# Kernel optimization log

Hardware: AMD Instinct MI355X
Metric: run time of the kernel (lower is better)

The kernel has to match this reference:

```python
import jax, jax.numpy as jnp
import numpy as np

N = 100000   # nodes
E = 600000   # edges
D = 128      # hidden_dim
R = 8        # edge_vocab_size (num_relations)
B = 64       # graphs in batch
V = 5000     # node_vocab_size
L = 3        # num_layers


def setup_inputs() -> dict:
    key = jax.random.key(0)
    ks = jax.random.split(key, 16)
    s = 1.0 / np.sqrt(D)
    node_type = jax.random.randint(ks[0], (N,), 0, V, dtype=jnp.int32)
    edge_index = jax.random.randint(ks[1], (2, E), 0, N, dtype=jnp.int32)
    edge_type = jax.random.randint(ks[2], (E,), 0, R, dtype=jnp.int32)
    batch = jnp.sort(jax.random.randint(ks[3], (N,), 0, B, dtype=jnp.int32))
    node_emb = jax.random.normal(ks[4], (V, D), dtype=jnp.float32)
    rel_w = jax.random.normal(ks[5], (L, R, D, D), dtype=jnp.float32) * s
    root_w = jax.random.normal(ks[6], (L, D, D), dtype=jnp.float32) * s
    bias = jnp.zeros((L, D), dtype=jnp.float32)
    risk_w1 = jax.random.normal(ks[7], (D, D), dtype=jnp.float32) * s
    risk_b1 = jnp.zeros((D,), dtype=jnp.float32)
    risk_w2 = jax.random.normal(ks[8], (D, 1), dtype=jnp.float32) * s
    risk_b2 = jnp.zeros((1,), dtype=jnp.float32)
    safe_w1 = jax.random.normal(ks[9], (D, D), dtype=jnp.float32) * s
    safe_b1 = jnp.zeros((D,), dtype=jnp.float32)
    safe_w2 = jax.random.normal(ks[10], (D, 1), dtype=jnp.float32) * s
    safe_b2 = jnp.zeros((1,), dtype=jnp.float32)
    return dict(node_type=node_type, edge_index=edge_index, edge_type=edge_type,
                batch=batch, node_emb=node_emb, rel_w=rel_w, root_w=root_w,
                bias=bias, risk_w1=risk_w1, risk_b1=risk_b1, risk_w2=risk_w2,
                risk_b2=risk_b2, safe_w1=safe_w1, safe_b1=safe_b1,
                safe_w2=safe_w2, safe_b2=safe_b2)


def _rgcn_layer(x, edge_index, edge_type, Wrel, Wroot, b):
    # PyG RGCNConv: per-relation mean aggregation of source features,
    # then relation-specific linear + root transform + bias.
    src, dst = edge_index[0], edge_index[1]
    seg = dst * R + edge_type                      # combined (node, relation) id
    msgs = x[src]                                  # [E, D] gather
    sums = jax.ops.segment_sum(msgs, seg, num_segments=N * R)      # [N*R, D]
    cnt = jax.ops.segment_sum(jnp.ones((E,), x.dtype), seg, num_segments=N * R)
    mean = sums / jnp.maximum(cnt, 1.0)[:, None]
    mean = mean.reshape(N, R, D)
    out = jnp.einsum('nrd,rde->ne', mean, Wrel) + x @ Wroot + b
    return out


def _mlp_head(g, w1, b1, w2, b2):
    h = jax.nn.relu(g @ w1 + b1)
    return (h @ w2 + b2).squeeze(-1)               # dropout is identity in eval


def reference(node_type, edge_index, edge_type, batch, node_emb, rel_w, root_w,
              bias, risk_w1, risk_b1, risk_w2, risk_b2, safe_w1, safe_b1,
              safe_w2, safe_b2):
    x = node_emb[node_type]                        # [N, D]
    for l in range(L):                             # fixed small layer loop
        x = jax.nn.relu(_rgcn_layer(x, edge_index, edge_type,
                                    rel_w[l], root_w[l], bias[l]))
    # global_mean_pool over graph ids
    g_sum = jax.ops.segment_sum(x, batch, num_segments=B)          # [B, D]
    g_cnt = jax.ops.segment_sum(jnp.ones((N,), x.dtype), batch, num_segments=B)
    g = g_sum / jnp.maximum(g_cnt, 1.0)[:, None]
    risk_pred = _mlp_head(g, risk_w1, risk_b1, risk_w2, risk_b2)   # [B]
    safe_logit = _mlp_head(g, safe_w1, safe_b1, safe_w2, safe_b2)  # [B]
    return risk_pred, safe_logit
```

## Files before the change

### kernel.cpp

```cpp
#include <hip/hip_runtime.h>
#include <hip/hip_bf16.h>

#define N_NODES 100000
#define N_EDGES 600000
#define DIM     128
#define N_REL   8
#define N_GRAPH 64
#define N_LAYER 3
#define NR      (N_NODES * N_REL)
#define NB1     782

typedef __attribute__((ext_vector_type(4))) float float4v;
typedef __attribute__((ext_vector_type(2))) float float2v;
typedef unsigned long long ull;

__device__ __forceinline__ int gswz8(int row, int g) {
    return row * 16 + (g ^ (row & 15));
}

#define W8_TOTAL (N_LAYER * 9 * 8192)
#define PB_HIST  2344
#define PB_GATH  12500
#define PB_WPRE  864
#define PB_BCNT  1
#define PB_TOTAL (PB_HIST + PB_GATH + PB_WPRE + PB_BCNT)

__global__ __launch_bounds__(256) void k_prep(
    const int* __restrict__ ei, const int* __restrict__ et, int* __restrict__ counts,
    const int* __restrict__ nt, const float* __restrict__ emb, unsigned int* __restrict__ x8,
    const float* __restrict__ relw, const float* __restrict__ rootw,
    unsigned short* __restrict__ W8,
    const int* __restrict__ batch, int* __restrict__ gcnt)
{
    const int b = blockIdx.x, t = threadIdx.x;
    if (b < PB_HIST) {
        int e = b * 256 + t;
        if (e < N_EDGES) {
            int seg = ei[N_EDGES + e] * N_REL + et[e];
            atomicAdd(&counts[seg], 1);
        }
    } else if (b < PB_HIST + PB_GATH) {
        int gid = (b - PB_HIST) * 256 + t;
        int n = gid >> 5, up = gid & 31;
        const float* row = emb + (size_t)nt[n] * DIM;
        int p0 = up * 4;
        float f0 = row[((p0 + 0) & 7) * 16 + ((p0 + 0) >> 3)];
        float f1 = row[((p0 + 1) & 7) * 16 + ((p0 + 1) >> 3)];
        float f2 = row[((p0 + 2) & 7) * 16 + ((p0 + 2) >> 3)];
        float f3 = row[((p0 + 3) & 7) * 16 + ((p0 + 3) >> 3)];
        int u = __builtin_amdgcn_cvt_pk_fp8_f32(f0, f1, 0, false);
        u = __builtin_amdgcn_cvt_pk_fp8_f32(f2, f3, u, true);
        x8[gid] = (unsigned int)u;
    } else if (b < PB_HIST + PB_GATH + PB_WPRE) {
        int gid = (b - PB_HIST - PB_GATH) * 256 + t;
        int l = gid / (9 * 8192);
        int rem = gid - l * 9 * 8192;
        int r = rem >> 13;
        int idx = rem & 8191;
        int n = idx >> 6, p2 = idx & 63;
        int pos0 = 2 * p2, pos1 = 2 * p2 + 1;
        int k0 = (pos0 & 7) * 16 + (pos0 >> 3);
        int k1 = (pos1 & 7) * 16 + (pos1 >> 3);
        float w0, w1;
        if (r < 8) {
            const float* base = relw + ((size_t)(l * 8 + r) * 128) * 128 + n;
            w0 = base[(size_t)k0 * 128];
            w1 = base[(size_t)k1 * 128];
        } else {
            const float* base = rootw + (size_t)l * 128 * 128 + n;
            w0 = base[(size_t)k0 * 128];
            w1 = base[(size_t)k1 * 128];
        }
        int pk = __builtin_amdgcn_cvt_pk_fp8_f32(w0, w1, 0, false);
        W8[gid] = (unsigned short)(pk & 0xffff);
    } else {
        int g = t;
        if (g < N_GRAPH) {
            int lo = 0, hi = N_NODES;
            while (lo < hi) { int mid = (lo + hi) >> 1; if (batch[mid] < g) lo = mid + 1; else hi = mid; }
            int start = lo;
            lo = 0; hi = N_NODES;
            while (lo < hi) { int mid = (lo + hi) >> 1; if (batch[mid] < g + 1) lo = mid + 1; else hi = mid; }
            gcnt[g] = lo - start;
        }
    }
}

__global__ __launch_bounds__(256) void k_scan1(const int* __restrict__ cnts,
                                               int* __restrict__ part,
                                               int* __restrict__ bsum) {
    __shared__ int sh[256];
    int t = threadIdx.x;
    int base = blockIdx.x * 1024 + t * 4;
    int v0 = (base + 0 < NR) ? cnts[base + 0] : 0;
    int v1 = (base + 1 < NR) ? cnts[base + 1] : 0;
    int v2 = (base + 2 < NR) ? cnts[base + 2] : 0;
    int v3 = (base + 3 < NR) ? cnts[base + 3] : 0;
    int tot = v0 + v1 + v2 + v3;
    sh[t] = tot;
    __syncthreads();
    for (int off = 1; off < 256; off <<= 1) {
        int x = (t >= off) ? sh[t - off] : 0;
        __syncthreads();
        sh[t] += x;
        __syncthreads();
    }
    int exc = sh[t] - tot;
    if (base + 0 < NR) part[base + 0] = exc;
    if (base + 1 < NR) part[base + 1] = exc + v0;
    if (base + 2 < NR) part[base + 2] = exc + v0 + v1;
    if (base + 3 < NR) part[base + 3] = exc + v0 + v1 + v2;
    if (t == 255) bsum[blockIdx.x] = sh[t];
}

__global__ __launch_bounds__(1024) void k_scan2(int* __restrict__ bsum, int nb) {
    __shared__ int sh[1024];
    int t = threadIdx.x;
    int v = (t < nb) ? bsum[t] : 0;
    sh[t] = v;
    __syncthreads();
    for (int off = 1; off < 1024; off <<= 1) {
        int x = (t >= off) ? sh[t - off] : 0;
        __syncthreads();
        sh[t] += x;
        __syncthreads();
    }
    if (t < nb) bsum[t] = sh[t] - v;
}

__global__ void k_scan3(const int* __restrict__ part, const int* __restrict__ bsum,
                        int* __restrict__ rowptr, int* __restrict__ cursor) {
    int i = blockIdx.x * 256 + threadIdx.x;
    if (i < NR) {
        int v = part[i] + bsum[i >> 10];
        rowptr[i] = v;
        cursor[i] = v;
    }
    if (i == 0) rowptr[NR] = N_EDGES;
}

__global__ void k_scatter(const int* __restrict__ ei, const int* __restrict__ et,
                          int* __restrict__ cursor, int* __restrict__ srcs) {
    int e = blockIdx.x * 256 + threadIdx.x;
    if (e < N_EDGES) {
        int seg = ei[N_EDGES + e] * N_REL + et[e];
        int p = atomicAdd(&cursor[seg], 1);
        srcs[p] = ei[e];
    }
}

__global__ __launch_bounds__(256) void k_agg(
    const unsigned int* __restrict__ x8,
    const int* __restrict__ rowptr,
    const int* __restrict__ srcs,
    unsigned int* __restrict__ Ag8,
    int d0, int rows, int srows)
{
    const int t = threadIdx.x;
    const int wv = t >> 6, lane = t & 63;
    const int q = lane >> 4, j = lane & 15;
    const int nb0 = (blockIdx.x * 4 + wv) * 4;
    if (nb0 >= rows) return;
    const int myn = nb0 + q;
    const bool nvalid = (myn < rows);

    int pr = 0;
    {
        int idx = (d0 + nb0) * 8 + lane;
        if (idx > NR) idx = NR;
        if (lane < 33) pr = rowptr[idx];
    }
    const int P0 = __shfl(pr, 0);
    const int Dtot = __shfl(pr, 32) - P0;

    int my_src = 0;
    if (lane < Dtot) my_src = srcs[P0 + lane];

    const uint2* x2p = (const uint2*)x8;
    uint2* Agf = (uint2*)Ag8;

    for (int r = 0; r < 8; ++r) {
        int e0 = __shfl(pr, q * 8 + r);
        int e1 = __shfl(pr, q * 8 + r + 1);
        int cnt = e1 - e0;
        int m1 = max(cnt, __shfl_xor(cnt, 16));
        int maxc = max(m1, __shfl_xor(m1, 32));
        float2v A0 = {0.f, 0.f}, A1 = {0.f, 0.f}, A2 = {0.f, 0.f}, A3 = {0.f, 0.f};
        int k = 0;
        for (; k + 2 <= maxc; k += 2) {
            int ei0 = e0 + k, ei1 = e0 + k + 1;
            int r0 = ei0 - P0, r1 = ei1 - P0;
            int s0 = __shfl(my_src, r0 & 63);
            int s1 = __shfl(my_src, r1 & 63);
            if (r0 >= 64) s0 = srcs[ei0];
            if (r1 >= 64) s1 = srcs[ei1];
            bool v0 = (k < cnt), v1 = (k + 1 < cnt);
            uint2 u0, u1;
            if (v0) u0 = x2p[(size_t)s0 * 16 + j];
            if (v1) u1 = x2p[(size_t)s1 * 16 + j];
            if (v0) {
                A0 += __builtin_amdgcn_cvt_pk_f32_fp8((int)u0.x, false);
                A1 += __builtin_amdgcn_cvt_pk_f32_fp8((int)u0.x, true);
                A2 += __builtin_amdgcn_cvt_pk_f32_fp8((int)u0.y, false);
                A3 += __builtin_amdgcn_cvt_pk_f32_fp8((int)u0.y, true);
            }
            if (v1) {
                A0 += __builtin_amdgcn_cvt_pk_f32_fp8((int)u1.x, false);
                A1 += __builtin_amdgcn_cvt_pk_f32_fp8((int)u1.x, true);
                A2 += __builtin_amdgcn_cvt_pk_f32_fp8((int)u1.y, false);
                A3 += __builtin_amdgcn_cvt_pk_f32_fp8((int)u1.y, true);
            }
        }
        if (k < maxc) {
            int ei = e0 + k;
            int ridx = ei - P0;
            int s = __shfl(my_src, ridx & 63);
            if (ridx >= 64) s = srcs[ei];
            if (k < cnt) {
                uint2 u = x2p[(size_t)s * 16 + j];
                A0 += __builtin_amdgcn_cvt_pk_f32_fp8((int)u.x, false);
                A1 += __builtin_amdgcn_cvt_pk_f32_fp8((int)u.x, true);
                A2 += __builtin_amdgcn_cvt_pk_f32_fp8((int)u.y, false);
                A3 += __builtin_amdgcn_cvt_pk_f32_fp8((int)u.y, true);
            }
        }
        float inv = (cnt > 0) ? 1.0f / (float)cnt : 0.f;
        float2v iv = {inv, inv};
        A0 *= iv; A1 *= iv; A2 *= iv; A3 *= iv;
        int u0 = __builtin_amdgcn_cvt_pk_fp8_f32(A0.x, A0.y, 0, false);
        u0 = __builtin_amdgcn_cvt_pk_fp8_f32(A1.x, A1.y, u0, true);
        int u1 = __builtin_amdgcn_cvt_pk_fp8_f32(A2.x, A2.y, 0, false);
        u1 = __builtin_amdgcn_cvt_pk_fp8_f32(A3.x, A3.y, u1, true);
        if (nvalid) {
            uint2 v; v.x = (unsigned int)u0; v.y = (unsigned int)u1;
            Agf[(size_t)r * srows * 16 + (size_t)(myn >> 4) * 256 + j * 16 + (myn & 15)] = v;
        }
    }
}

#define BM2 128
__global__ __launch_bounds__(256) void k_gemm(
    const unsigned int* __restrict__ Ag8,
    const unsigned int* __restrict__ x8in,
    unsigned int* __restrict__ x8out,
    const unsigned short* __restrict__ W8,
    const float* __restrict__ bias,
    int d0, int srows)
{
    __shared__ __align__(16) ull Bls[4096];
    const int t = threadIdx.x;
    const int wv = t >> 6, lane = t & 63;
    const int quad = lane >> 4, l15 = lane & 15;
    const int m0 = d0 + blockIdx.x * BM2;

    float4v acc[2][8];
#pragma unroll
    for (int nt = 0; nt < 8; ++nt) {
        float bc = bias[nt * 16 + l15];
        acc[0][nt] = (float4v){bc, bc, bc, bc};
        acc[1][nt] = (float4v){bc, bc, bc, bc};
    }

    const size_t pstride = (size_t)srows * 16;
    const ull* Ag = (const ull*)Ag8 + ((size_t)((m0 - d0) >> 4) + 2 * wv) * 256;
    const ull* Xr = (const ull*)x8in;

    ull aC[8], aN[8], bR[8];
    {
        const ull* Wc = (const ull*)W8;
#pragma unroll
        for (int i = 0; i < 8; ++i) {
            aC[i] = Ag[(size_t)(i >> 2) * 256 + (i & 3) * 64 + lane];
            bR[i] = Wc[t + 256 * i];
        }
    }
#pragma unroll
    for (int i = 0; i < 8; ++i) {
        int idx = t + 256 * i;
        Bls[gswz8(idx >> 4, idx & 15)] = bR[i];
    }
    __syncthreads();

    for (int c = 0; c < 9; ++c) {
        const int cur = (c & 1) * 2048;
        if (c < 8) {
            if (c + 1 < 8) {
                const ull* Ac = Ag + (size_t)(c + 1) * pstride;
#pragma unroll
                for (int i = 0; i < 8; ++i)
                    aN[i] = Ac[(size_t)(i >> 2) * 256 + (i & 3) * 64 + lane];
            } else {
#pragma unroll
                for (int i = 0; i < 8; ++i) {
                    int rt = i >> 2, kk = i & 3;
                    aN[i] = Xr[(size_t)(m0 + wv * 32 + rt * 16 + l15) * 16 + kk * 4 + quad];
                }
            }
            const ull* Wc = (const ull*)(W8 + (size_t)(c + 1) * 8192);
#pragma unroll
            for (int i = 0; i < 8; ++i) bR[i] = Wc[t + 256 * i];
        }
#pragma unroll
        for (int kk = 0; kk < 4; ++kk) {
            long long a0 = (long long)aC[kk];
            long long a1 = (long long)aC[4 + kk];
            int g = kk * 4 + quad;
#pragma unroll
            for (int nt = 0; nt < 8; ++nt) {
                long long b8 = (long long)Bls[cur + (nt * 16 + l15) * 16 + (g ^ l15)];
                acc[0][nt] = __builtin_amdgcn_mfma_f32_16x16x32_fp8_fp8(a0, b8, acc[0][nt], 0, 0, 0);
                acc[1][nt] = __builtin_amdgcn_mfma_f32_16x16x32_fp8_fp8(a1, b8, acc[1][nt], 0, 0, 0);
            }
        }
        if (c < 8) {
            const int nxt = ((c + 1) & 1) * 2048;
#pragma unroll
            for (int i = 0; i < 8; ++i) {
                int idx = t + 256 * i;
                Bls[nxt + gswz8(idx >> 4, idx & 15)] = bR[i];
                aC[i] = aN[i];
            }
            __syncthreads();
        }
    }
    ull* outs = (ull*)x8out;
#pragma unroll
    for (int rt = 0; rt < 2; ++rt) {
#pragma unroll
        for (int i = 0; i < 4; ++i) {
            int row = m0 + wv * 32 + rt * 16 + quad * 4 + i;
            float v0 = acc[rt][0][i], v1 = acc[rt][1][i];
            float v2 = acc[rt][2][i], v3 = acc[rt][3][i];
            float v4 = acc[rt][4][i], v5 = acc[rt][5][i];
            float v6 = acc[rt][6][i], v7 = acc[rt][7][i];
            v0 = v0 > 0.f ? v0 : 0.f;  v1 = v1 > 0.f ? v1 : 0.f;
            v2 = v2 > 0.f ? v2 : 0.f;  v3 = v3 > 0.f ? v3 : 0.f;
            v4 = v4 > 0.f ? v4 : 0.f;  v5 = v5 > 0.f ? v5 : 0.f;
            v6 = v6 > 0.f ? v6 : 0.f;  v7 = v7 > 0.f ? v7 : 0.f;
            int lo = __builtin_amdgcn_cvt_pk_fp8_f32(v0, v1, 0, false);
            lo = __builtin_amdgcn_cvt_pk_fp8_f32(v2, v3, lo, true);
            int hi = __builtin_amdgcn_cvt_pk_fp8_f32(v4, v5, 0, false);
            hi = __builtin_amdgcn_cvt_pk_fp8_f32(v6, v7, hi, true);
            if (row < N_NODES) {
                ull w = ((ull)(unsigned int)hi << 32) | (unsigned int)lo;
                outs[(size_t)row * 16 + l15] = w;
            }
        }
    }
}

__global__ __launch_bounds__(256) void k_pool(const unsigned int* __restrict__ x8,
                                              const int* __restrict__ batch,
                                              float* __restrict__ gsum) {
    const int wv = threadIdx.x >> 6, lane = threadIdx.x & 63;
    const int n0 = (blockIdx.x * 4 + wv) * 64;
    if (n0 >= N_NODES) return;
    int n1 = n0 + 64;
    if (n1 > N_NODES) n1 = N_NODES;
    const int nb = n1 - n0;
    const unsigned short* xs = (const unsigned short*)x8;
    int bb = batch[n0 + (lane < nb ? lane : nb - 1)];
    float2v A = {0.f, 0.f};
    int cur = __shfl(bb, 0);
    for (int base = 0; base < nb; base += 8) {
        unsigned int u[8];
        int m = nb - base;
#pragma unroll
        for (int qq = 0; qq < 8; ++qq)
            if (qq < m) u[qq] = xs[(size_t)(n0 + base + qq) * 64 + lane];
#pragma unroll
        for (int qq = 0; qq < 8; ++qq) {
            if (qq < m) {
                int b = __shfl(bb, base + qq);
                if (b != cur) {
                    atomicAdd(&gsum[cur * 128 + lane * 2], A.x);
                    atomicAdd(&gsum[cur * 128 + lane * 2 + 1], A.y);
                    A = (float2v){0.f, 0.f};
                    cur = b;
                }
                A += __builtin_amdgcn_cvt_pk_f32_fp8((int)u[qq], false);
            }
        }
    }
    atomicAdd(&gsum[cur * 128 + lane * 2], A.x);
    atomicAdd(&gsum[cur * 128 + lane * 2 + 1], A.y);
}

__global__ __launch_bounds__(128) void k_heads(
    const float* __restrict__ gsum, const int* __restrict__ gcnt,
    const float* __restrict__ rw1, const float* __restrict__ rb1,
    const float* __restrict__ rw2, const float* __restrict__ rb2,
    const float* __restrict__ sw1, const float* __restrict__ sb1,
    const float* __restrict__ sw2, const float* __restrict__ sb2,
    float* __restrict__ out) {
    __shared__ float g[128];
    __shared__ float parts[2];
    int b = blockIdx.x, t = threadIdx.x;
    int c = gcnt[b];
    float invc = 1.0f / (float)(c > 0 ? c : 1);
    g[((t & 7) << 4) | (t >> 3)] = gsum[b * 128 + t] * invc;
    __syncthreads();
    float acc = rb1[t];
    for (int d = 0; d < 128; ++d) acc += g[d] * rw1[d * 128 + t];
    float h = acc > 0.f ? acc : 0.f;
    float p = h * rw2[t];
    for (int o = 32; o > 0; o >>= 1) p += __shfl_down(p, o);
    if ((t & 63) == 0) parts[t >> 6] = p;
    __syncthreads();
    if (t == 0) out[b] = parts[0] + parts[1] + rb2[0];
    __syncthreads();
    acc = sb1[t];
    for (int d = 0; d < 128; ++d) acc += g[d] * sw1[d * 128 + t];
    h = acc > 0.f ? acc : 0.f;
    p = h * sw2[t];
    for (int o = 32; o > 0; o >>= 1) p += __shfl_down(p, o);
    if ((t & 63) == 0) parts[t >> 6] = p;
    __syncthreads();
    if (t == 0) out[64 + b] = parts[0] + parts[1] + sb2[0];
}

extern "C" void kernel_launch(void* const* d_in, const int* in_sizes, int n_in,
                              void* d_out, int out_size, void* d_ws, size_t ws_size,
                              hipStream_t stream) {
    const int*   node_type  = (const int*)d_in[0];
    const int*   edge_index = (const int*)d_in[1];
    const int*   edge_type  = (const int*)d_in[2];
    const int*   batch      = (const int*)d_in[3];
    const float* node_emb   = (const float*)d_in[4];
    const float* rel_w      = (const float*)d_in[5];
    const float* root_w     = (const float*)d_in[6];
    const float* bias       = (const float*)d_in[7];
    const float* rw1        = (const float*)d_in[8];
    const float* rb1        = (const float*)d_in[9];
    const float* rw2        = (const float*)d_in[10];
    const float* rb2        = (const float*)d_in[11];
    const float* sw1        = (const float*)d_in[12];
    const float* sb1        = (const float*)d_in[13];
    const float* sw2        = (const float*)d_in[14];
    const float* sb2        = (const float*)d_in[15];
    float* out = (float*)d_out;

    char* ws = (char*)d_ws;
    size_t off = 0;
    auto alloc = [&](size_t bytes) -> void* {
        void* p = ws + off;
        off += (bytes + 255) & ~(size_t)255;
        return p;
    };
    unsigned int*   x8a    = (unsigned int*)alloc((size_t)N_NODES * 32 * 4);
    unsigned int*   x8b    = (unsigned int*)alloc((size_t)N_NODES * 32 * 4);
    int*            rowptr = (int*)alloc((size_t)(NR + 1) * 4);
    int*            srcs   = (int*)alloc((size_t)N_EDGES * 4);
    int*            bsum   = (int*)alloc(1024 * 4);
    unsigned short* W8     = (unsigned short*)alloc((size_t)W8_TOTAL * 2);
    float*          gsum   = (float*)alloc((64 * 128 + 64) * 4);
    int*            gcnt   = (int*)(gsum + 64 * 128);
    size_t off_common = off;
    int*            cursor = (int*)alloc((size_t)NR * 4);
    int*            counts = (int*)alloc((size_t)NR * 4);
    size_t off_sort = off;
    if (off_sort > ws_size) return;
    unsigned int*   Ag8    = (unsigned int*)(ws + off_common);
    size_t avail = ws_size - off_common;
    long max_rows = (avail > 32768) ? (long)((avail - 32768) / 1024) : 0;
    int srows = (int)((max_rows / 128) * 128);
    if (srows > N_NODES + 127) srows = ((N_NODES + 127) / 128) * 128;
    if (srows < 128) return;

    hipMemsetAsync(counts, 0, (size_t)NR * 4, stream);
    hipMemsetAsync(gsum, 0, (size_t)(64 * 128 + 64) * 4, stream);
    k_prep<<<PB_TOTAL, 256, 0, stream>>>(edge_index, edge_type, counts,
                                         node_type, node_emb, x8a,
                                         rel_w, root_w, W8, batch, gcnt);
    k_scan1<<<NB1, 256, 0, stream>>>(counts, cursor, bsum);
    k_scan2<<<1, 1024, 0, stream>>>(bsum, NB1);
    k_scan3<<<(NR + 255) / 256, 256, 0, stream>>>(cursor, bsum, rowptr, cursor);
    k_scatter<<<(N_EDGES + 255) / 256, 256, 0, stream>>>(edge_index, edge_type, cursor, srcs);

    unsigned int* xcur = x8a;
    unsigned int* xnext = x8b;
    for (int l = 0; l < N_LAYER; ++l) {
        const unsigned short* W8l = W8 + (size_t)l * 9 * 8192;
        const float* bl = bias + (size_t)l * 128;
        for (int d0 = 0; d0 < N_NODES; d0 += srows) {
            int rows = N_NODES - d0;
            if (rows > srows) rows = srows;
            int ab = (rows + 15) / 16;
            int gb = (rows + BM2 - 1) / BM2;
            k_agg<<<ab, 256, 0, stream>>>(xcur, rowptr, srcs, Ag8, d0, rows, srows);
            k_gemm<<<gb, 256, 0, stream>>>(Ag8, xcur, xnext, W8l, bl, d0, srows);
        }
        unsigned int* tmp = xcur; xcur = xnext; xnext = tmp;
    }

    k_pool<<<(N_NODES + 255) / 256, 256, 0, stream>>>(xcur, batch, gsum);
    k_heads<<<64, 128, 0, stream>>>(gsum, gcnt, rw1, rb1, rw2, rb2,
                                    sw1, sb1, sw2, sb2, out);
}
```

Measured before the change: 419.0 us.

## Fuse per-relation mean aggregation into the RGCN GEMM kernel via LDS

Removes the separate aggregation kernel and its fp8 intermediate buffer. The GEMM kernel now gathers and averages neighbor features for each relation chunk itself, writes them into a swizzled LDS tile, and overlaps the next relation's gather with the current MFMA chunk. The global write and re-read of the aggregated tensor and one launch per layer go away, in exchange for more work, registers and LDS in the GEMM kernel, with gather latency now on its critical path. The gather also switches to 16-byte loads with 8 lanes per node, and the workspace-based row chunking is dropped.

Result: slower. 458.6 us (+9.5%).

```diff
diff --git a/kernel.cpp b/kernel.cpp
--- a/kernel.cpp
+++ b/kernel.cpp
@@ -149,109 +149,22 @@
     }
 }
 
-__global__ __launch_bounds__(256) void k_agg(
-    const unsigned int* __restrict__ x8,
-    const int* __restrict__ rowptr,
-    const int* __restrict__ srcs,
-    unsigned int* __restrict__ Ag8,
-    int d0, int rows, int srows)
-{
-    const int t = threadIdx.x;
-    const int wv = t >> 6, lane = t & 63;
-    const int q = lane >> 4, j = lane & 15;
-    const int nb0 = (blockIdx.x * 4 + wv) * 4;
-    if (nb0 >= rows) return;
-    const int myn = nb0 + q;
-    const bool nvalid = (myn < rows);
-
-    int pr = 0;
-    {
-        int idx = (d0 + nb0) * 8 + lane;
-        if (idx > NR) idx = NR;
-        if (lane < 33) pr = rowptr[idx];
-    }
-    const int P0 = __shfl(pr, 0);
-    const int Dtot = __shfl(pr, 32) - P0;
-
-    int my_src = 0;
-    if (lane < Dtot) my_src = srcs[P0 + lane];
-
-    const uint2* x2p = (const uint2*)x8;
-    uint2* Agf = (uint2*)Ag8;
-
-    for (int r = 0; r < 8; ++r) {
-        int e0 = __shfl(pr, q * 8 + r);
-        int e1 = __shfl(pr, q * 8 + r + 1);
-        int cnt = e1 - e0;
-        int m1 = max(cnt, __shfl_xor(cnt, 16));
-        int maxc = max(m1, __shfl_xor(m1, 32));
-        float2v A0 = {0.f, 0.f}, A1 = {0.f, 0.f}, A2 = {0.f, 0.f}, A3 = {0.f, 0.f};
-        int k = 0;
-        for (; k + 2 <= maxc; k += 2) {
-            int ei0 = e0 + k, ei1 = e0 + k + 1;
-            int r0 = ei0 - P0, r1 = ei1 - P0;
-            int s0 = __shfl(my_src, r0 & 63);
-            int s1 = __shfl(my_src, r1 & 63);
-            if (r0 >= 64) s0 = srcs[ei0];
-            if (r1 >= 64) s1 = srcs[ei1];
-            bool v0 = (k < cnt), v1 = (k + 1 < cnt);
-            uint2 u0, u1;
-            if (v0) u0 = x2p[(size_t)s0 * 16 + j];
-            if (v1) u1 = x2p[(size_t)s1 * 16 + j];
-            if (v0) {
-                A0 += __builtin_amdgcn_cvt_pk_f32_fp8((int)u0.x, false);
-                A1 += __builtin_amdgcn_cvt_pk_f32_fp8((int)u0.x, true);
-                A2 += __builtin_amdgcn_cvt_pk_f32_fp8((int)u0.y, false);
-                A3 += __builtin_amdgcn_cvt_pk_f32_fp8((int)u0.y, true);
-            }
-            if (v1) {
-                A0 += __builtin_amdgcn_cvt_pk_f32_fp8((int)u1.x, false);
-                A1 += __builtin_amdgcn_cvt_pk_f32_fp8((int)u1.x, true);
-                A2 += __builtin_amdgcn_cvt_pk_f32_fp8((int)u1.y, false);
-                A3 += __builtin_amdgcn_cvt_pk_f32_fp8((int)u1.y, true);
-            }
-        }
-        if (k < maxc) {
-            int ei = e0 + k;
-            int ridx = ei - P0;
-            int s = __shfl(my_src, ridx & 63);
-            if (ridx >= 64) s = srcs[ei];
-            if (k < cnt) {
-                uint2 u = x2p[(size_t)s * 16 + j];
-                A0 += __builtin_amdgcn_cvt_pk_f32_fp8((int)u.x, false);
-                A1 += __builtin_amdgcn_cvt_pk_f32_fp8((int)u.x, true);
-                A2 += __builtin_amdgcn_cvt_pk_f32_fp8((int)u.y, false);
-                A3 += __builtin_amdgcn_cvt_pk_f32_fp8((int)u.y, true);
-            }
-        }
-        float inv = (cnt > 0) ? 1.0f / (float)cnt : 0.f;
-        float2v iv = {inv, inv};
-        A0 *= iv; A1 *= iv; A2 *= iv; A3 *= iv;
-        int u0 = __builtin_amdgcn_cvt_pk_fp8_f32(A0.x, A0.y, 0, false);
-        u0 = __builtin_amdgcn_cvt_pk_fp8_f32(A1.x, A1.y, u0, true);
-        int u1 = __builtin_amdgcn_cvt_pk_fp8_f32(A2.x, A2.y, 0, false);
-        u1 = __builtin_amdgcn_cvt_pk_fp8_f32(A3.x, A3.y, u1, true);
-        if (nvalid) {
-            uint2 v; v.x = (unsigned int)u0; v.y = (unsigned int)u1;
-            Agf[(size_t)r * srows * 16 + (size_t)(myn >> 4) * 256 + j * 16 + (myn & 15)] = v;
-        }
-    }
-}
-
 #define BM2 128
 __global__ __launch_bounds__(256) void k_gemm(
-    const unsigned int* __restrict__ Ag8,
     const unsigned int* __restrict__ x8in,
     unsigned int* __restrict__ x8out,
     const unsigned short* __restrict__ W8,
     const float* __restrict__ bias,
-    int d0, int srows)
+    const int* __restrict__ rowptr,
+    const int* __restrict__ srcs)
 {
     __shared__ __align__(16) ull Bls[4096];
+    __shared__ __align__(16) ull Als[2048];
     const int t = threadIdx.x;
     const int wv = t >> 6, lane = t & 63;
     const int quad = lane >> 4, l15 = lane & 15;
-    const int m0 = d0 + blockIdx.x * BM2;
+    const int oct = lane >> 3, h = lane & 7;
+    const int m0 = blockIdx.x * BM2;
 
     float4v acc[2][8];
 #pragma unroll
@@ -261,18 +174,87 @@
         acc[1][nt] = (float4v){bc, bc, bc, bc};
     }
 
-    const size_t pstride = (size_t)srows * 16;
-    const ull* Ag = (const ull*)Ag8 + ((size_t)((m0 - d0) >> 4) + 2 * wv) * 256;
     const ull* Xr = (const ull*)x8in;
-
-    ull aC[8], aN[8], bR[8];
+    const uint4* x4p = (const uint4*)x8in;
+    ull* AlsW = Als + wv * 512;
+    uint4* Als4 = (uint4*)AlsW;
+
+    ull bR[8], aR[8];
+
+#define ACCUM(U) do {                                                  \
+        A0 += __builtin_amdgcn_cvt_pk_f32_fp8((int)(U).x, false);      \
+        A1 += __builtin_amdgcn_cvt_pk_f32_fp8((int)(U).x, true);       \
+        A2 += __builtin_amdgcn_cvt_pk_f32_fp8((int)(U).y, false);      \
+        A3 += __builtin_amdgcn_cvt_pk_f32_fp8((int)(U).y, true);       \
+        A4 += __builtin_amdgcn_cvt_pk_f32_fp8((int)(U).z, false);      \
+        A5 += __builtin_amdgcn_cvt_pk_f32_fp8((int)(U).z, true);       \
+        A6 += __builtin_amdgcn_cvt_pk_f32_fp8((int)(U).w, false);      \
+        A7 += __builtin_amdgcn_cvt_pk_f32_fp8((int)(U).w, true);       \
+    } while (0)
+
+    auto aggv = [&](int rr) -> int {
+        int gn = m0 + wv * 32 + (lane >> 1);
+        int idxp = (gn < N_NODES) ? gn * 8 + rr + (lane & 1) : NR;
+        return rowptr[idxp];
+    };
+
+    auto aggrest = [&](int val) {
+        int f = lane & 1;
+        int e0l = __shfl(val, lane & 62);
+        int cl  = __shfl(val, lane | 1) - e0l;
+        int sl  = (f < cl) ? srcs[e0l + f] : 0;
+        uint4 u0[4], u1[4];
+        int cc[4], eb[4];
+#pragma unroll
+        for (int nn = 0; nn < 4; ++nn) {
+            int lw = nn * 8 + oct;
+            int e0 = __shfl(val, lw * 2);
+            int e1 = __shfl(val, lw * 2 + 1);
+            int s0 = __shfl(sl, lw * 2);
+            int s1 = __shfl(sl, lw * 2 + 1);
+            cc[nn] = e1 - e0; eb[nn] = e0;
+            if (cc[nn] > 0) u0[nn] = x4p[(size_t)s0 * 8 + h];
+            if (cc[nn] > 1) u1[nn] = x4p[(size_t)s1 * 8 + h];
+        }
+#pragma unroll
+        for (int nn = 0; nn < 4; ++nn) {
+            int lw = nn * 8 + oct;
+            float2v A0 = {0.f, 0.f}, A1 = {0.f, 0.f}, A2 = {0.f, 0.f}, A3 = {0.f, 0.f};
+            float2v A4 = {0.f, 0.f}, A5 = {0.f, 0.f}, A6 = {0.f, 0.f}, A7 = {0.f, 0.f};
+            if (cc[nn] > 0) ACCUM(u0[nn]);
+            if (cc[nn] > 1) ACCUM(u1[nn]);
+#pragma unroll 1
+            for (int k = 2; k < cc[nn]; ++k) {
+                int s = srcs[eb[nn] + k];
+                uint4 uu = x4p[(size_t)s * 8 + h];
+                ACCUM(uu);
+            }
+            float inv = (cc[nn] > 0) ? 1.0f / (float)cc[nn] : 0.f;
+            float2v iv = {inv, inv};
+            A0 *= iv; A1 *= iv; A2 *= iv; A3 *= iv;
+            A4 *= iv; A5 *= iv; A6 *= iv; A7 *= iv;
+            int w0 = __builtin_amdgcn_cvt_pk_fp8_f32(A0.x, A0.y, 0, false);
+            w0 = __builtin_amdgcn_cvt_pk_fp8_f32(A1.x, A1.y, w0, true);
+            int w1 = __builtin_amdgcn_cvt_pk_fp8_f32(A2.x, A2.y, 0, false);
+            w1 = __builtin_amdgcn_cvt_pk_fp8_f32(A3.x, A3.y, w1, true);
+            int w2 = __builtin_amdgcn_cvt_pk_fp8_f32(A4.x, A4.y, 0, false);
+            w2 = __builtin_amdgcn_cvt_pk_fp8_f32(A5.x, A5.y, w2, true);
+            int w3 = __builtin_amdgcn_cvt_pk_fp8_f32(A6.x, A6.y, 0, false);
+            w3 = __builtin_amdgcn_cvt_pk_fp8_f32(A7.x, A7.y, w3, true);
+            uint4 w; w.x = (unsigned int)w0; w.y = (unsigned int)w1;
+            w.z = (unsigned int)w2; w.w = (unsigned int)w3;
+            Als4[(lw >> 4) * 128 + h * 16 + ((lw & 15) ^ h)] = w;
+        }
+    };
+
     {
         const ull* Wc = (const ull*)W8;
 #pragma unroll
-        for (int i = 0; i < 8; ++i) {
-            aC[i] = Ag[(size_t)(i >> 2) * 256 + (i & 3) * 64 + lane];
-            bR[i] = Wc[t + 256 * i];
-        }
+        for (int i = 0; i < 8; ++i) bR[i] = Wc[t + 256 * i];
+    }
+    {
+        int v0 = aggv(0);
+        aggrest(v0);
     }
 #pragma unroll
     for (int i = 0; i < 8; ++i) {
@@ -283,27 +265,33 @@
 
     for (int c = 0; c < 9; ++c) {
         const int cur = (c & 1) * 2048;
+        int val = 0;
+        if (c < 7) val = aggv(c + 1);
         if (c < 8) {
-            if (c + 1 < 8) {
-                const ull* Ac = Ag + (size_t)(c + 1) * pstride;
-#pragma unroll
-                for (int i = 0; i < 8; ++i)
-                    aN[i] = Ac[(size_t)(i >> 2) * 256 + (i & 3) * 64 + lane];
+            const ull* Wc = (const ull*)(W8 + (size_t)(c + 1) * 8192);
+#pragma unroll
+            for (int i = 0; i < 8; ++i) bR[i] = Wc[t + 256 * i];
+        }
+        if (c == 7) {
+#pragma unroll
+            for (int i = 0; i < 8; ++i) {
+                int rt = i >> 2, kk = i & 3;
+                aR[i] = Xr[(size_t)(m0 + wv * 32 + rt * 16 + l15) * 16 + kk * 4 + quad];
+            }
+        }
+#pragma unroll
+        for (int kk = 0; kk < 4; ++kk) {
+            long long a0, a1;
+            if (c == 8) {
+                a0 = (long long)aR[kk];
+                a1 = (long long)aR[4 + kk];
             } else {
-#pragma unroll
-                for (int i = 0; i < 8; ++i) {
-                    int rt = i >> 2, kk = i & 3;
-                    aN[i] = Xr[(size_t)(m0 + wv * 32 + rt * 16 + l15) * 16 + kk * 4 + quad];
-                }
-            }
-            const ull* Wc = (const ull*)(W8 + (size_t)(c + 1) * 8192);
-#pragma unroll
-            for (int i = 0; i < 8; ++i) bR[i] = Wc[t + 256 * i];
-        }
-#pragma unroll
-        for (int kk = 0; kk < 4; ++kk) {
-            long long a0 = (long long)aC[kk];
-            long long a1 = (long long)aC[4 + kk];
+                int j4 = kk * 4 + quad;
+                int h2 = j4 >> 1, hf = j4 & 1;
+                int slot = ((h2 * 16 + (l15 ^ h2)) << 1) | hf;
+                a0 = (long long)AlsW[slot];
+                a1 = (long long)AlsW[256 + slot];
+            }
             int g = kk * 4 + quad;
 #pragma unroll
             for (int nt = 0; nt < 8; ++nt) {
@@ -318,11 +306,13 @@
             for (int i = 0; i < 8; ++i) {
                 int idx = t + 256 * i;
                 Bls[nxt + gswz8(idx >> 4, idx & 15)] = bR[i];
-                aC[i] = aN[i];
-            }
+            }
+            if (c < 7) aggrest(val);
             __syncthreads();
         }
     }
+#undef ACCUM
+
     ull* outs = (ull*)x8out;
 #pragma unroll
     for (int rt = 0; rt < 2; ++rt) {
@@ -455,17 +445,9 @@
     unsigned short* W8     = (unsigned short*)alloc((size_t)W8_TOTAL * 2);
     float*          gsum   = (float*)alloc((64 * 128 + 64) * 4);
     int*            gcnt   = (int*)(gsum + 64 * 128);
-    size_t off_common = off;
     int*            cursor = (int*)alloc((size_t)NR * 4);
     int*            counts = (int*)alloc((size_t)NR * 4);
-    size_t off_sort = off;
-    if (off_sort > ws_size) return;
-    unsigned int*   Ag8    = (unsigned int*)(ws + off_common);
-    size_t avail = ws_size - off_common;
-    long max_rows = (avail > 32768) ? (long)((avail - 32768) / 1024) : 0;
-    int srows = (int)((max_rows / 128) * 128);
-    if (srows > N_NODES + 127) srows = ((N_NODES + 127) / 128) * 128;
-    if (srows < 128) return;
+    if (off > ws_size) return;
 
     hipMemsetAsync(counts, 0, (size_t)NR * 4, stream);
     hipMemsetAsync(gsum, 0, (size_t)(64 * 128 + 64) * 4, stream);
@@ -479,17 +461,11 @@
 
     unsigned int* xcur = x8a;
     unsigned int* xnext = x8b;
+    const int gb = (N_NODES + BM2 - 1) / BM2;
     for (int l = 0; l < N_LAYER; ++l) {
         const unsigned short* W8l = W8 + (size_t)l * 9 * 8192;
         const float* bl = bias + (size_t)l * 128;
-        for (int d0 = 0; d0 < N_NODES; d0 += srows) {
-            int rows = N_NODES - d0;
-            if (rows > srows) rows = srows;
-            int ab = (rows + 15) / 16;
-            int gb = (rows + BM2 - 1) / BM2;
-            k_agg<<<ab, 256, 0, stream>>>(xcur, rowptr, srcs, Ag8, d0, rows, srows);
-            k_gemm<<<gb, 256, 0, stream>>>(Ag8, xcur, xnext, W8l, bl, d0, srows);
-        }
+        k_gemm<<<gb, 256, 0, stream>>>(xcur, xnext, W8l, bl, rowptr, srcs);
         unsigned int* tmp = xcur; xcur = xnext; xnext = tmp;
     }
 
```
